# Optimization experiments

Measured on AMD Instinct MI355X. Metric: run time of the kernel, lower is better.

The kernel has to match this reference:

```python
import jax, jax.numpy as jnp
import numpy as np

BIG_NEGATIVE_SCALAR = -10000.0
SEGMENT_SIZE = 64
DILATION = 2
D_K = 128
POS_EMB_SCALING = 1.0


def setup_inputs() -> dict:
    key = jax.random.key(0)
    k1, k2, k3, k4, k5 = jax.random.split(key, 5)
    B, T, E = 4, 8192, 1024
    d_k, d_v = 128, 128
    inv = 1.0 / np.sqrt(d_k)
    return {
        "x_in": jax.random.normal(k1, (B, T, E), dtype=jnp.float32),
        "P": jax.random.normal(k2, (T, T), dtype=jnp.float32),
        "Wk": jax.random.normal(k3, (d_k, E), dtype=jnp.float32) * inv,
        "Wq": jax.random.normal(k4, (d_k, E), dtype=jnp.float32) * inv,
        "Wv": jax.random.normal(k5, (d_v, E), dtype=jnp.float32) * inv,
    }


def reference(x_in, P, Wk, Wq, Wv):
    B, T, E = x_in.shape
    seg, dil = SEGMENT_SIZE, DILATION
    nseg = T // seg
    norm_fact = 1.0 / np.sqrt(D_K)
    d_v = Wv.shape[0]

    # [B, nseg, seg, E] -> [B, seg, E, nseg], then dilate along the segment axis
    x_view = x_in.reshape(B, nseg, seg, E).transpose(0, 2, 3, 1)
    x_dil = x_view[:, :, :, ::dil]                      # [B, seg, E, nseg_d]

    Q = jnp.einsum('ijkl,mk->ijlm', x_dil, Wq)          # [B, seg, nseg_d, d_k]
    K = jnp.einsum('ijkl,mk->ijlm', x_dil, Wk)
    V = jnp.einsum('ijkl,mk->ijlm', x_dil, Wv)          # [B, seg, nseg_d, d_v]

    KQ = jnp.einsum('ijkp,ijop->ijko', K, Q)            # [B, seg, nseg_d(key), nseg_d(query)]

    causal_mask = jnp.tril(jnp.ones((nseg, nseg), dtype=bool))[::dil, ::dil]
    KQ = jnp.where(causal_mask, KQ, BIG_NEGATIVE_SCALAR)

    # positional bias: P is [T, T]; segment-level bias at within-segment offset 0
    Ps = P * POS_EMB_SCALING
    p_bias = Ps.reshape(nseg, seg, nseg, seg)[::dil, :, ::dil, :][:, 0, :, 0]
    KQ = KQ + p_bias

    smKQ = jax.nn.softmax(KQ * norm_fact, axis=2)       # softmax over key axis
    att = jnp.einsum('ijld,ijlm->ijdm', smKQ, V)        # [B, seg, nseg_d, d_v]

    # 'same' padding: scatter dilated outputs back into full-length sequence
    res = jnp.zeros((B, T, d_v), dtype=x_in.dtype)
    res = res.at[:, ::dil, :].set(att.reshape(B, -1, d_v))
    return res
```

## Files before the change

kernel.cpp:

```cpp
#include <hip/hip_runtime.h>

#define B_  4
#define T_  8192
#define E_  1024
#define DK_ 128

typedef __attribute__((ext_vector_type(8))) _Float16 half8;
typedef __attribute__((ext_vector_type(4))) float float4v;

__device__ __forceinline__ half8 cvt8h(float4 a, float4 b) {
    half8 r;
    r[0] = (_Float16)a.x; r[1] = (_Float16)a.y; r[2] = (_Float16)a.z; r[3] = (_Float16)a.w;
    r[4] = (_Float16)b.x; r[5] = (_Float16)b.y; r[6] = (_Float16)b.z; r[7] = (_Float16)b.w;
    return r;
}

__global__ void wconv(const float* __restrict__ Wk, const float* __restrict__ Wq,
                      const float* __restrict__ Wv, ushort* __restrict__ W16) {
    const int g   = blockIdx.x * 256 + threadIdx.x;
    const int c   = g & 7;
    const int ki  = (g >> 3) & 15;
    const int row = g >> 7;
    const float* src = (row < 128) ? (Wq + (size_t)row * E_)
                     : (row < 256) ? (Wk + (size_t)(row - 128) * E_)
                                   : (Wv + (size_t)(row - 256) * E_);
    src += ki * 64 + c * 8;
    *(half8*)(W16 + (size_t)(ki * 384 + row) * 64 + c * 8) =
        cvt8h(*(const float4*)src, *(const float4*)(src + 4));
}

__global__ __launch_bounds__(512, 2)
void dilattn(const float* __restrict__ x_in, const float* __restrict__ P,
             const ushort* __restrict__ W16, float* __restrict__ out)
{
    __shared__ float lds_f[16384];
    ushort* xs  = (ushort*)lds_f;
    ushort* wsm = xs + 64 * 72;
    constexpr int A_OFF = 0;
    constexpr int B_OFF = 8192;
    constexpr int S_OFF = 8192;
    const float NORMF = 0.08838834764831845f;

    const int tid  = threadIdx.x;
    const int lane = tid & 63;
    const int w    = __builtin_amdgcn_readfirstlane(tid >> 6);
    const int b    = blockIdx.x >> 6;
    const int s    = blockIdx.x & 63;

    const int lr   = lane & 15;
    const int lg   = lane >> 4;
    const int mt   = w & 3;
    const int half = w >> 2;

    const int c8 = tid & 7;
    const int xr = tid >> 3;
    const float*  xrow = x_in + ((size_t)b * T_ + 128 * xr + s) * E_ + c8 * 8;
    const ushort* wrow = W16 + xr * 64 + c8 * 8;

    float4v acc[12];
#pragma unroll
    for (int j = 0; j < 12; ++j) acc[j] = (float4v){0.f, 0.f, 0.f, 0.f};

    float4 xa0, xa1;
    uint4  wa[6];
    xa0 = *(const float4*)(xrow);
    xa1 = *(const float4*)(xrow + 4);
#pragma unroll
    for (int p = 0; p < 6; ++p) wa[p] = *(const uint4*)(wrow + p * 4096);

    for (int ki = 0; ki < 16; ++ki) {
        __syncthreads();
        *(half8*)&xs[xr * 72 + c8 * 8] = cvt8h(xa0, xa1);
#pragma unroll
        for (int p = 0; p < 6; ++p)
            *(uint4*)&wsm[(xr + 64 * p) * 72 + c8 * 8] = wa[p];
        __syncthreads();

        if (ki < 15) {
            const int k0 = (ki + 1) * 64;
            xa0 = *(const float4*)(xrow + k0);
            xa1 = *(const float4*)(xrow + k0 + 4);
            const int wk = (ki + 1) * 24576;
#pragma unroll
            for (int p = 0; p < 6; ++p)
                wa[p] = *(const uint4*)(wrow + wk + p * 4096);
        }

#pragma unroll
        for (int kk = 0; kk < 2; ++kk) {
            const half8 afr = *(const half8*)&xs[(mt * 16 + lr) * 72 + kk * 32 + lg * 8];
#pragma unroll
            for (int j = 0; j < 12; ++j) {
                const half8 bfr = *(const half8*)&wsm[((half * 12 + j) * 16 + lr) * 72 + kk * 32 + lg * 8];
                acc[j] = __builtin_amdgcn_mfma_f32_16x16x32_f16(afr, bfr, acc[j], 0, 0, 0);
            }
        }
    }
    __syncthreads();

    const int rbase = mt * 16 + lg * 4;
#pragma unroll
    for (int j = 0; j < 12; ++j) {
        const int nt = half * 12 + j;
        const int n  = nt * 16 + lr;
        if (nt < 8) {
#pragma unroll
            for (int r = 0; r < 4; ++r) {
                const int l = rbase + r;
                lds_f[A_OFF + l * 128 + ((n + 4 * l) & 127)] = acc[j][r];
            }
        } else if (nt < 16) {
            const int m = n - 128;
#pragma unroll
            for (int r = 0; r < 4; ++r) {
                const int l = rbase + r;
                lds_f[B_OFF + m * 64 + ((l + m) & 63)] = acc[j][r];
            }
        }
    }
    __syncthreads();

    float pb[8];
#pragma unroll
    for (int i = 0; i < 8; ++i)
        pb[i] = P[(size_t)lane * ((size_t)128 * T_) + (size_t)(w * 8 + i) * 128];

    float sd[8];
#pragma unroll
    for (int i = 0; i < 8; ++i) sd[i] = 0.f;

    for (int m4 = 0; m4 < 32; ++m4) {
        const int mm = 4 * m4;
        const float k0 = lds_f[B_OFF + (mm + 0) * 64 + ((lane + mm + 0) & 63)];
        const float k1 = lds_f[B_OFF + (mm + 1) * 64 + ((lane + mm + 1) & 63)];
        const float k2 = lds_f[B_OFF + (mm + 2) * 64 + ((lane + mm + 2) & 63)];
        const float k3 = lds_f[B_OFF + (mm + 3) * 64 + ((lane + mm + 3) & 63)];
#pragma unroll
        for (int i = 0; i < 8; ++i) {
            const int q = w * 8 + i;
            const float4 qv = *(const float4*)&lds_f[A_OFF + q * 128 + ((4 * (m4 + q)) & 127)];
            sd[i] = fmaf(k0, qv.x, fmaf(k1, qv.y, fmaf(k2, qv.z, fmaf(k3, qv.w, sd[i]))));
        }
    }
    __syncthreads();

    if (half == 1) {
#pragma unroll
        for (int j = 4; j < 12; ++j) {
            const int nt = 12 + j;
            const int m  = nt * 16 + lr - 256;
#pragma unroll
            for (int r = 0; r < 4; ++r) {
                const int l = rbase + r;
                lds_f[A_OFF + l * 128 + ((m + 4 * l) & 127)] = acc[j][r];
            }
        }
    }

#pragma unroll
    for (int i = 0; i < 8; ++i) {
        const int q = w * 8 + i;
        const float logit = ((lane >= q ? sd[i] : -10000.f) + pb[i]) * NORMF;
        float mx = logit;
#pragma unroll
        for (int off = 32; off >= 1; off >>= 1) mx = fmaxf(mx, __shfl_xor(mx, off));
        const float ev = __expf(logit - mx);
        float sum = ev;
#pragma unroll
        for (int off = 32; off >= 1; off >>= 1) sum += __shfl_xor(sum, off);
        lds_f[S_OFF + lane * 65 + q] = ev * (1.0f / sum);
    }
    __syncthreads();

    float4 o0 = {0,0,0,0}, o1 = {0,0,0,0}, o2 = {0,0,0,0}, o3 = {0,0,0,0};
    for (int k = 0; k < 64; ++k) {
        const float p = lds_f[S_OFF + k * 65 + lane];
        const int base = A_OFF + k * 128;
        const float4 v0 = *(const float4*)&lds_f[base + ((16 * w + 0  + 4 * k) & 127)];
        const float4 v1 = *(const float4*)&lds_f[base + ((16 * w + 4  + 4 * k) & 127)];
        const float4 v2 = *(const float4*)&lds_f[base + ((16 * w + 8  + 4 * k) & 127)];
        const float4 v3 = *(const float4*)&lds_f[base + ((16 * w + 12 + 4 * k) & 127)];
        o0.x = fmaf(p, v0.x, o0.x); o0.y = fmaf(p, v0.y, o0.y); o0.z = fmaf(p, v0.z, o0.z); o0.w = fmaf(p, v0.w, o0.w);
        o1.x = fmaf(p, v1.x, o1.x); o1.y = fmaf(p, v1.y, o1.y); o1.z = fmaf(p, v1.z, o1.z); o1.w = fmaf(p, v1.w, o1.w);
        o2.x = fmaf(p, v2.x, o2.x); o2.y = fmaf(p, v2.y, o2.y); o2.z = fmaf(p, v2.z, o2.z); o2.w = fmaf(p, v2.w, o2.w);
        o3.x = fmaf(p, v3.x, o3.x); o3.y = fmaf(p, v3.y, o3.y); o3.z = fmaf(p, v3.z, o3.z); o3.w = fmaf(p, v3.w, o3.w);
    }
    float* orow = out + ((size_t)b * T_ + (size_t)(2 * (s * 64 + lane))) * DK_ + w * 16;
    *(float4*)(orow + 0)  = o0;
    *(float4*)(orow + 4)  = o1;
    *(float4*)(orow + 8)  = o2;
    *(float4*)(orow + 12) = o3;
}

extern "C" void kernel_launch(void* const* d_in, const int* in_sizes, int n_in,
                              void* d_out, int out_size, void* d_ws, size_t ws_size,
                              hipStream_t stream) {
    (void)in_sizes; (void)n_in; (void)ws_size;
    const float* x_in = (const float*)d_in[0];
    const float* P    = (const float*)d_in[1];
    const float* Wk   = (const float*)d_in[2];
    const float* Wq   = (const float*)d_in[3];
    const float* Wv   = (const float*)d_in[4];
    float* out = (float*)d_out;
    ushort* W16 = (ushort*)d_ws;

    hipMemsetAsync(d_out, 0, (size_t)out_size * sizeof(float), stream);
    wconv<<<dim3(192), dim3(256), 0, stream>>>(Wk, Wq, Wv, W16);
    dilattn<<<dim3(256), dim3(512), 0, stream>>>(x_in, P, W16, out);
}
```

Baseline: 468.1 us.

## Fuse weight conversion and output zeroing into main attention kernel

Removes the separate weight fp16 conversion kernel and the output memset. The main kernel now loads fp32 weights directly and converts them to fp16 while staging into LDS, and each thread writes zeros to the odd (non-dilated) output rows it owns. This cuts two launches and a full 16 MB memset pass, in exchange for doubling the weight global-load bytes per block and adding conversion work inside the K loop.

```diff
diff --git a/kernel.cpp b/kernel.cpp
--- a/kernel.cpp
+++ b/kernel.cpp
@@ -15,23 +15,10 @@
     return r;
 }
 
-__global__ void wconv(const float* __restrict__ Wk, const float* __restrict__ Wq,
-                      const float* __restrict__ Wv, ushort* __restrict__ W16) {
-    const int g   = blockIdx.x * 256 + threadIdx.x;
-    const int c   = g & 7;
-    const int ki  = (g >> 3) & 15;
-    const int row = g >> 7;
-    const float* src = (row < 128) ? (Wq + (size_t)row * E_)
-                     : (row < 256) ? (Wk + (size_t)(row - 128) * E_)
-                                   : (Wv + (size_t)(row - 256) * E_);
-    src += ki * 64 + c * 8;
-    *(half8*)(W16 + (size_t)(ki * 384 + row) * 64 + c * 8) =
-        cvt8h(*(const float4*)src, *(const float4*)(src + 4));
-}
-
 __global__ __launch_bounds__(512, 2)
 void dilattn(const float* __restrict__ x_in, const float* __restrict__ P,
-             const ushort* __restrict__ W16, float* __restrict__ out)
+             const float* __restrict__ Wk, const float* __restrict__ Wq,
+             const float* __restrict__ Wv, float* __restrict__ out)
 {
     __shared__ float lds_f[16384];
     ushort* xs  = (ushort*)lds_f;
@@ -54,36 +41,47 @@
 
     const int c8 = tid & 7;
     const int xr = tid >> 3;
-    const float*  xrow = x_in + ((size_t)b * T_ + 128 * xr + s) * E_ + c8 * 8;
-    const ushort* wrow = W16 + xr * 64 + c8 * 8;
+    const float* xrow = x_in + ((size_t)b * T_ + 128 * xr + s) * E_ + c8 * 8;
+    const float* wrow[6];
+#pragma unroll
+    for (int p = 0; p < 6; ++p) {
+        const int r = xr + 64 * p;
+        const float* base = (r < 128) ? (Wq + (size_t)r * E_)
+                          : (r < 256) ? (Wk + (size_t)(r - 128) * E_)
+                                      : (Wv + (size_t)(r - 256) * E_);
+        wrow[p] = base + c8 * 8;
+    }
 
     float4v acc[12];
 #pragma unroll
     for (int j = 0; j < 12; ++j) acc[j] = (float4v){0.f, 0.f, 0.f, 0.f};
 
-    float4 xa0, xa1;
-    uint4  wa[6];
+    float4 xa0, xa1, wa0[6], wa1[6];
     xa0 = *(const float4*)(xrow);
     xa1 = *(const float4*)(xrow + 4);
 #pragma unroll
-    for (int p = 0; p < 6; ++p) wa[p] = *(const uint4*)(wrow + p * 4096);
+    for (int p = 0; p < 6; ++p) {
+        wa0[p] = *(const float4*)(wrow[p]);
+        wa1[p] = *(const float4*)(wrow[p] + 4);
+    }
 
     for (int ki = 0; ki < 16; ++ki) {
         __syncthreads();
         *(half8*)&xs[xr * 72 + c8 * 8] = cvt8h(xa0, xa1);
 #pragma unroll
         for (int p = 0; p < 6; ++p)
-            *(uint4*)&wsm[(xr + 64 * p) * 72 + c8 * 8] = wa[p];
+            *(half8*)&wsm[(xr + 64 * p) * 72 + c8 * 8] = cvt8h(wa0[p], wa1[p]);
         __syncthreads();
 
         if (ki < 15) {
             const int k0 = (ki + 1) * 64;
             xa0 = *(const float4*)(xrow + k0);
             xa1 = *(const float4*)(xrow + k0 + 4);
-            const int wk = (ki + 1) * 24576;
-#pragma unroll
-            for (int p = 0; p < 6; ++p)
-                wa[p] = *(const uint4*)(wrow + wk + p * 4096);
+#pragma unroll
+            for (int p = 0; p < 6; ++p) {
+                wa0[p] = *(const float4*)(wrow[p] + k0);
+                wa1[p] = *(const float4*)(wrow[p] + k0 + 4);
+            }
         }
 
 #pragma unroll
@@ -190,21 +188,23 @@
     *(float4*)(orow + 4)  = o1;
     *(float4*)(orow + 8)  = o2;
     *(float4*)(orow + 12) = o3;
+    const float4 z = {0.f, 0.f, 0.f, 0.f};
+    *(float4*)(orow + DK_ + 0)  = z;
+    *(float4*)(orow + DK_ + 4)  = z;
+    *(float4*)(orow + DK_ + 8)  = z;
+    *(float4*)(orow + DK_ + 12) = z;
 }
 
 extern "C" void kernel_launch(void* const* d_in, const int* in_sizes, int n_in,
                               void* d_out, int out_size, void* d_ws, size_t ws_size,
                               hipStream_t stream) {
-    (void)in_sizes; (void)n_in; (void)ws_size;
+    (void)in_sizes; (void)n_in; (void)out_size; (void)d_ws; (void)ws_size;
     const float* x_in = (const float*)d_in[0];
     const float* P    = (const float*)d_in[1];
     const float* Wk   = (const float*)d_in[2];
     const float* Wq   = (const float*)d_in[3];
     const float* Wv   = (const float*)d_in[4];
     float* out = (float*)d_out;
-    ushort* W16 = (ushort*)d_ws;
-
-    hipMemsetAsync(d_out, 0, (size_t)out_size * sizeof(float), stream);
-    wconv<<<dim3(192), dim3(256), 0, stream>>>(Wk, Wq, Wv, W16);
-    dilattn<<<dim3(256), dim3(512), 0, stream>>>(x_in, P, W16, out);
+
+    dilattn<<<dim3(256), dim3(512), 0, stream>>>(x_in, P, Wk, Wq, Wv, out);
 }
```

Result: faster. 436.0 us (-6.9%).
